# Kernel tuning notes

Hardware: AMD Instinct MI355X
Metric: run time of the kernel (lower is better)

Reference implementation:

```python
import jax, jax.numpy as jnp
import numpy as np

SEED_SPACING = 0.06      # eps for DBSCAN
MIN_SAMPLES = 3          # sklearn counts the point itself
MAX_SUPERPOINTS = 512


def _dbscan_superpoints(coords):
    """DBSCAN(eps, min_samples=3) on [N,3] coords + the module's relabeling.

    Connected components over the eps-graph restricted to core points are
    found by min-index label propagation (with pointer jumping) inside a
    while_loop; border points take the min core-neighbor label; noise is
    filled with the most common label; labels are compacted and capped at
    MAX_SUPERPOINTS exactly as in the torch module. Returns [N] int32.
    """
    N = coords.shape[0]
    SENT = N  # sentinel label meaning "no cluster / noise"

    # pairwise squared euclidean distances via GEMM
    sq = jnp.sum(coords * coords, axis=-1)                      # [N]
    d2 = sq[:, None] + sq[None, :] - 2.0 * (coords @ coords.T)  # [N,N]
    adj = d2 <= SEED_SPACING * SEED_SPACING                     # includes self
    core = jnp.sum(adj, axis=-1) >= MIN_SAMPLES                 # [N] bool

    idx = jnp.arange(N)
    core_col = core[None, :]

    def step(l):
        # min label among core neighbors
        nb = jnp.min(jnp.where(adj & core_col, l[None, :], SENT), axis=-1)
        l2 = jnp.where(core, jnp.minimum(l, nb), SENT)
        # pointer jumping: labels are indices of core points, so l2[l2] is valid
        safe = jnp.where(l2 < N, l2, 0)
        l2 = jnp.where(l2 < N, jnp.minimum(l2, l2[safe]), SENT)
        return l2

    def cond(state):
        return state[1]

    def body(state):
        l, _ = state
        l_new = step(l)
        return l_new, jnp.any(l_new != l)

    l0 = jnp.where(core, idx, SENT)
    l_final, _ = jax.lax.while_loop(cond, body, (l0, jnp.array(True)))

    # border points: min label of any core neighbor; else stay noise
    border = jnp.min(jnp.where(adj & core_col, l_final[None, :], SENT), axis=-1)
    labels = jnp.where(core, l_final, border)

    # noise fill: assign most common valid label (or 0 if none valid)
    noise = labels == SENT
    safe_lab = jnp.where(noise, 0, labels)
    counts = jnp.zeros(N, jnp.int32).at[safe_lab].add(jnp.where(noise, 0, 1))
    any_valid = jnp.any(~noise)
    most_common = jnp.argmax(counts).astype(labels.dtype)
    labels = jnp.where(noise, jnp.where(any_valid, most_common, 0), labels)

    # compact to consecutive ids ordered by min point index (== first occurrence)
    present = jnp.zeros(N, bool).at[labels].set(True)
    rank = (jnp.cumsum(present) - 1).astype(labels.dtype)
    labels = rank[labels]
    n_clusters = jnp.sum(present)

    # cap at MAX_SUPERPOINTS: keep the MAX largest clusters, rest -> 0
    counts2 = jnp.zeros(N, jnp.int32).at[labels].add(1)
    top = jnp.argsort(counts2)[-MAX_SUPERPOINTS:]
    remap = jnp.zeros(N, labels.dtype).at[top].set(
        jnp.arange(MAX_SUPERPOINTS, dtype=labels.dtype))
    labels = jnp.where(n_clusters > MAX_SUPERPOINTS, remap[labels], labels)
    return labels.astype(jnp.int32)


def setup_inputs() -> dict:
    key = jax.random.key(0)
    coordinates = jax.random.uniform(key, (8, 4096, 3), dtype=jnp.float32)
    return {"coordinates": coordinates}


def reference(coordinates):
    # [B, N, 3] -> [B, N] int32 superpoint labels
    return jax.vmap(_dbscan_superpoints)(coordinates)
```

## Files before the change

kernel.cpp:

```cpp
#include <hip/hip_runtime.h>
#include <stdint.h>

#define NPTS 4096
#define SENT NPTS
#define MAXSP 512
#define SCAP 1024
#define NSLICE 32
#define ESLOTS (SCAP*NSLICE)
#define ECACHE 16384

typedef unsigned long long ull;

__device__ __forceinline__ int find_lds(int* p, int x){
  while (true){
    int px = p[x];
    if (px == x) return x;
    int ppx = p[px];
    if (ppx == px) return px;
    p[x] = ppx;
    x = ppx;
  }
}

__device__ __forceinline__ void union_lds(int* p, int a, int b){
  a = find_lds(p, a);
  b = find_lds(p, b);
  while (a != b){
    int lo = min(a, b), hi = max(a, b);
    int old = atomicCAS(&p[hi], hi, lo);
    if (old == hi || old == lo) return;
    a = lo; b = old;
  }
}

__device__ __forceinline__ ull trimask(ull m, int i, int base){
  if (base + 63 <= i) return 0ULL;
  if (base <= i) return m & ((~0ULL) << (i - base + 1));
  return m;
}

__device__ __forceinline__ float4 loadpt(const float* __restrict__ c, int g){
#pragma clang fp contract(off)
  float x = c[g*3+0], y = c[g*3+1], z = c[g*3+2];
  float sq = ((x*x) + (y*y)) + (z*z);
  return make_float4(x, y, z, sq);
}

__global__ __launch_bounds__(1024) void k_adj(const float* __restrict__ coords,
                                              uint32_t* __restrict__ edges,
                                              int* __restrict__ scnt,
                                              int* __restrict__ rcnt){
#pragma clang fp contract(off)
  __shared__ float4 P[NPTS];
  __shared__ int sTot;
  int tid  = threadIdx.x;
  int wid  = tid >> 6, lane = tid & 63;
  int b     = blockIdx.x >> 5;
  int slice = blockIdx.x & 31;
  int u512  = (slice << 4) + wid;
  int i0 = u512 << 2;
  int h0 = (NPTS - 4) - i0;
  const float* cb = coords + ((size_t)b << 12) * 3;
  if (tid == 0) sTot = 0;
  for (int g = tid; g < NPTS; g += 1024) P[g] = loadpt(cb, g);
  __syncthreads();
  const float EPS2 = (float)(0.06 * 0.06);
  float4 pL[4], pH[4];
  #pragma unroll
  for (int r = 0; r < 4; ++r){ pL[r] = P[i0 + r]; pH[r] = P[h0 + r]; }
  ull wl[4] = {0,0,0,0}, wh[4] = {0,0,0,0};
  int base = lane << 6;
  {
    int W = i0 >> 6;
    for (int k = W; k < 64; ++k){
      float4 cur = P[(k << 6) + lane];
      #pragma unroll
      for (int r = 0; r < 4; ++r){
        float dot = __builtin_fmaf(pL[r].z, cur.z,
                    __builtin_fmaf(pL[r].y, cur.y, pL[r].x * cur.x));
        float d2  = __builtin_fmaf(-2.0f, dot, pL[r].w + cur.w);
        ull bal = __ballot(d2 <= EPS2);
        if (lane == k) wl[r] = bal;
      }
    }
  }
  {
    int W = h0 >> 6;
    for (int k = W; k < 64; ++k){
      float4 cur = P[(k << 6) + lane];
      #pragma unroll
      for (int r = 0; r < 4; ++r){
        float dot = __builtin_fmaf(pH[r].z, cur.z,
                    __builtin_fmaf(pH[r].y, cur.y, pH[r].x * cur.x));
        float d2  = __builtin_fmaf(-2.0f, dot, pH[r].w + cur.w);
        ull bal = __ballot(d2 <= EPS2);
        if (lane == k) wh[r] = bal;
      }
    }
  }
  int* rc = rcnt + (b << 12);
  #pragma unroll
  for (int r = 0; r < 4; ++r){
    wl[r] = trimask(wl[r], i0 + r, base);
    wh[r] = trimask(wh[r], h0 + r, base);
    int cl = __popcll(wl[r]), ch = __popcll(wh[r]);
    #pragma unroll
    for (int off = 32; off; off >>= 1){
      cl += __shfl_xor(cl, off);
      ch += __shfl_xor(ch, off);
    }
    if (lane == 0){ rc[i0 + r] = cl; rc[h0 + r] = ch; }
  }
  int cnt = 0;
  #pragma unroll
  for (int r = 0; r < 4; ++r) cnt += __popcll(wl[r]) + __popcll(wh[r]);
  int incl = cnt;
  #pragma unroll
  for (int off = 1; off < 64; off <<= 1){
    int y = __shfl_up(incl, off);
    if (lane >= off) incl += y;
  }
  int total = __shfl(incl, 63);
  int woff = 0;
  if (lane == 63) woff = atomicAdd(&sTot, total);
  woff = __shfl(woff, 63);
  __syncthreads();
  if (tid == 0) scnt[(b << 5) + slice] = min(sTot, SCAP);
  int pos = woff + incl - cnt;
  uint32_t* eb = edges + (size_t)b * ESLOTS + slice * SCAP;
  #define EMIT(mm, row) { ull e = (mm); while (e){ int bit = __builtin_ctzll(e); \
      e &= e - 1; if (pos < SCAP) eb[pos] = ((uint32_t)(row) << 12) | (uint32_t)(base + bit); ++pos; } }
  #pragma unroll
  for (int r = 0; r < 4; ++r) EMIT(wl[r], i0 + r)
  #pragma unroll
  for (int r = 0; r < 4; ++r) EMIT(wh[r], h0 + r)
  #undef EMIT
}

__global__ __launch_bounds__(1024) void k_mega(const uint32_t* __restrict__ edges,
                                               const int* __restrict__ scnt,
                                               const int* __restrict__ rcnt,
                                               uint32_t* __restrict__ spill,
                                               int* __restrict__ out){
  __shared__ int par[NPTS];
  __shared__ int LAB[NPTS];
  __shared__ int Bb[NPTS];
  __shared__ unsigned char corea[NPTS];
  __shared__ uint32_t ec[ECACHE];
  __shared__ int pref[NSLICE + 1];
  __shared__ int wtots[16];
  __shared__ int sMost;
  int b = blockIdx.x, t = threadIdx.x;
  int wid = t >> 6, lane = t & 63;
  const uint32_t* eb = edges + (size_t)b * ESLOTS;
  const int* rc = rcnt + (b << 12);
  uint32_t* sp = spill + (size_t)b * (ESLOTS - ECACHE);
  if (t < NSLICE) pref[t + 1] = scnt[(b << 5) + t];
  if (t == 0){ pref[0] = 0; sMost = -1; }
  for (int s = 0; s < 4; ++s){ int v = (t << 2) + s; par[v] = rc[v]; }
  __syncthreads();
  for (int off = 1; off < NSLICE; off <<= 1){
    int v = 0;
    if (t < NSLICE && t >= off) v = pref[t + 1 - off];
    __syncthreads();
    if (t < NSLICE && t >= off) pref[t + 1] += v;
    __syncthreads();
  }
  int cnt = pref[NSLICE];
  for (int d = t; d < cnt; d += 1024){
    int lo = 0, hi = NSLICE - 1;
    #pragma unroll
    for (int s = 0; s < 5; ++s){
      int mid = (lo + hi) >> 1;
      if (pref[mid + 1] <= d) lo = mid + 1; else hi = mid;
    }
    uint32_t pk = eb[(lo << 10) + (d - pref[lo])];
    if (d < ECACHE) ec[d] = pk; else sp[d - ECACHE] = pk;
    atomicAdd(&par[pk & 4095], 1);
  }
  __syncthreads();
  for (int s = 0; s < 4; ++s){ int v = (t << 2) + s; corea[v] = (par[v] >= 2) ? 1 : 0; }
  __syncthreads();
  for (int s = 0; s < 4; ++s){ int v = (t << 2) + s; par[v] = v; }
  __syncthreads();
  for (int d = t; d < cnt; d += 1024){
    uint32_t pk = (d < ECACHE) ? ec[d] : sp[d - ECACHE];
    int u = pk >> 12, v = pk & 4095;
    if (corea[u] && corea[v]) union_lds(par, u, v);
  }
  __syncthreads();
  for (int s = 0; s < 4; ++s){
    int v = (t << 2) + s;
    LAB[v] = corea[v] ? find_lds(par, v) : SENT;
  }
  __syncthreads();
  for (int d = t; d < cnt; d += 1024){
    uint32_t pk = (d < ECACHE) ? ec[d] : sp[d - ECACHE];
    int u = pk >> 12, v = pk & 4095;
    int cu = corea[u], cv = corea[v];
    if (cu && !cv)      atomicMin(&LAB[v], find_lds(par, u));
    else if (cv && !cu) atomicMin(&LAB[u], find_lds(par, v));
  }
  __syncthreads();
  int* A = par;
  for (int s = 0; s < 4; ++s){ int v = (t << 2) + s; A[v] = 0; }
  __syncthreads();
  for (int s = 0; s < 4; ++s){ int l = LAB[(t << 2) + s]; if (l < SENT) atomicAdd(&A[l], 1); }
  __syncthreads();
  {
    int best = -1;
    for (int s = 0; s < 4; ++s){
      int v = (t << 2) + s; int c = A[v];
      if (c > 0) best = max(best, (c << 13) | (4095 - v));
    }
    #pragma unroll
    for (int off = 32; off; off >>= 1) best = max(best, __shfl_xor(best, off));
    if (lane == 0 && best >= 0) atomicMax(&sMost, best);
  }
  __syncthreads();
  int most = (sMost >= 0) ? (4095 - (sMost & 8191)) : 0;
  for (int s = 0; s < 4; ++s){ int v = (t << 2) + s; if (LAB[v] == SENT) LAB[v] = most; Bb[v] = 0; }
  __syncthreads();
  for (int s = 0; s < 4; ++s) Bb[LAB[(t << 2) + s]] = 1;
  __syncthreads();
  int pv[4]; int ls = 0;
  for (int s = 0; s < 4; ++s){ pv[s] = Bb[(t << 2) + s]; ls += pv[s]; }
  int incl = ls;
  #pragma unroll
  for (int off = 1; off < 64; off <<= 1){
    int y = __shfl_up(incl, off);
    if (lane >= off) incl += y;
  }
  if (lane == 63) wtots[wid] = incl;
  __syncthreads();
  int wbase = 0, ncl = 0;
  #pragma unroll
  for (int w = 0; w < 16; ++w){
    int wt = wtots[w];
    if (w < wid) wbase += wt;
    ncl += wt;
  }
  int run = wbase + incl - ls;
  for (int s = 0; s < 4; ++s){ run += pv[s]; Bb[(t << 2) + s] = run - 1; }
  __syncthreads();
  for (int s = 0; s < 4; ++s){ int v = (t << 2) + s; LAB[v] = Bb[LAB[v]]; }
  __syncthreads();
  if (ncl > MAXSP){
    for (int s = 0; s < 4; ++s) A[(t << 2) + s] = 0;
    __syncthreads();
    for (int s = 0; s < 4; ++s) atomicAdd(&A[LAB[(t << 2) + s]], 1);
    __syncthreads();
    for (int v = t; v < ncl; v += 1024){
      int keyv = A[v] * NPTS + v;
      int p = 0;
      for (int u = 0; u < ncl; ++u) p += ((A[u] * NPTS + u) < keyv) ? 1 : 0;
      int full = p + (NPTS - ncl);
      Bb[v] = (full >= NPTS - MAXSP) ? (full - (NPTS - MAXSP)) : 0;
    }
    __syncthreads();
    for (int s = 0; s < 4; ++s){ int v = (t << 2) + s; LAB[v] = Bb[LAB[v]]; }
    __syncthreads();
  }
  int* og = out + (b << 12);
  for (int s = 0; s < 4; ++s){ int v = (t << 2) + s; og[v] = LAB[v]; }
}

extern "C" void kernel_launch(void* const* d_in, const int* in_sizes, int n_in,
                              void* d_out, int out_size, void* d_ws, size_t ws_size,
                              hipStream_t stream){
  const float* coords = (const float*)d_in[0];
  int* out = (int*)d_out;
  int batches = in_sizes[0] / (NPTS * 3);

  char* ws = (char*)d_ws;
  size_t off = 0;
  int* scnt = (int*)(ws + off); off += (size_t)batches * NSLICE * sizeof(int);
  int* rcnt = (int*)(ws + off); off += (size_t)batches * NPTS * sizeof(int);
  uint32_t* edges = (uint32_t*)(ws + off); off += (size_t)batches * ESLOTS * sizeof(uint32_t);
  uint32_t* spill = (uint32_t*)(ws + off); off += (size_t)batches * (ESLOTS - ECACHE) * sizeof(uint32_t);

  k_adj<<<batches * NSLICE, 1024, 0, stream>>>(coords, edges, scnt, rcnt);
  k_mega<<<batches, 1024, 0, stream>>>(edges, scnt, rcnt, spill, out);
}
```

Baseline: 55.32 us.

## Fuse adjacency and clustering kernels via last-block-done counter per batch

Merges the edge-building kernel and the per-batch clustering kernel into one launch. Each slice block increments a per-batch atomic counter, and the last of the 32 blocks to finish runs the union-find, labeling and compaction phase, reusing the same shared memory regions. This removes a kernel launch and the gap between the two stages. In exchange, the LDS edge cache shrinks, so more edges spill to global memory. The counter is never reset and relies on a modulo-32 test, so correctness across repeated calls depends on the workspace state.

```diff
diff --git a/kernel.cpp b/kernel.cpp
--- a/kernel.cpp
+++ b/kernel.cpp
@@ -7,7 +7,7 @@
 #define SCAP 1024
 #define NSLICE 32
 #define ESLOTS (SCAP*NSLICE)
-#define ECACHE 16384
+#define ECLDS 10752
 
 typedef unsigned long long ull;
 
@@ -46,13 +46,16 @@
   return make_float4(x, y, z, sq);
 }
 
-__global__ __launch_bounds__(1024) void k_adj(const float* __restrict__ coords,
-                                              uint32_t* __restrict__ edges,
-                                              int* __restrict__ scnt,
-                                              int* __restrict__ rcnt){
+__global__ __launch_bounds__(1024, 8) void k_all(const float* __restrict__ coords,
+                                                 uint32_t* __restrict__ edges,
+                                                 int* __restrict__ scnt,
+                                                 int* __restrict__ rcnt,
+                                                 uint32_t* __restrict__ spill,
+                                                 unsigned int* __restrict__ ctr,
+                                                 int* __restrict__ out){
 #pragma clang fp contract(off)
-  __shared__ float4 P[NPTS];
-  __shared__ int sTot;
+  __shared__ float4 R1[NPTS];
+  __shared__ int    R2[NPTS];
   int tid  = threadIdx.x;
   int wid  = tid >> 6, lane = tid & 63;
   int b     = blockIdx.x >> 5;
@@ -61,19 +64,19 @@
   int i0 = u512 << 2;
   int h0 = (NPTS - 4) - i0;
   const float* cb = coords + ((size_t)b << 12) * 3;
-  if (tid == 0) sTot = 0;
-  for (int g = tid; g < NPTS; g += 1024) P[g] = loadpt(cb, g);
+  if (tid == 0) R2[0] = 0;
+  for (int g = tid; g < NPTS; g += 1024) R1[g] = loadpt(cb, g);
   __syncthreads();
   const float EPS2 = (float)(0.06 * 0.06);
-  float4 pL[4], pH[4];
-  #pragma unroll
-  for (int r = 0; r < 4; ++r){ pL[r] = P[i0 + r]; pH[r] = P[h0 + r]; }
-  ull wl[4] = {0,0,0,0}, wh[4] = {0,0,0,0};
   int base = lane << 6;
+  ull wl[4], wh[4];
+  float4 pL[4];
+  #pragma unroll
+  for (int r = 0; r < 4; ++r){ pL[r] = R1[i0 + r]; wl[r] = 0ULL; }
   {
     int W = i0 >> 6;
     for (int k = W; k < 64; ++k){
-      float4 cur = P[(k << 6) + lane];
+      float4 cur = R1[(k << 6) + lane];
       #pragma unroll
       for (int r = 0; r < 4; ++r){
         float dot = __builtin_fmaf(pL[r].z, cur.z,
@@ -85,9 +88,12 @@
     }
   }
   {
+    float4 pH[4];
+    #pragma unroll
+    for (int r = 0; r < 4; ++r){ pH[r] = R1[h0 + r]; wh[r] = 0ULL; }
     int W = h0 >> 6;
     for (int k = W; k < 64; ++k){
-      float4 cur = P[(k << 6) + lane];
+      float4 cur = R1[(k << 6) + lane];
       #pragma unroll
       for (int r = 0; r < 4; ++r){
         float dot = __builtin_fmaf(pH[r].z, cur.z,
@@ -122,10 +128,10 @@
   }
   int total = __shfl(incl, 63);
   int woff = 0;
-  if (lane == 63) woff = atomicAdd(&sTot, total);
+  if (lane == 63) woff = atomicAdd(&R2[0], total);
   woff = __shfl(woff, 63);
   __syncthreads();
-  if (tid == 0) scnt[(b << 5) + slice] = min(sTot, SCAP);
+  if (tid == 0) scnt[(b << 5) + slice] = min(R2[0], SCAP);
   int pos = woff + incl - cnt;
   uint32_t* eb = edges + (size_t)b * ESLOTS + slice * SCAP;
   #define EMIT(mm, row) { ull e = (mm); while (e){ int bit = __builtin_ctzll(e); \
@@ -135,28 +141,31 @@
   #pragma unroll
   for (int r = 0; r < 4; ++r) EMIT(wh[r], h0 + r)
   #undef EMIT
-}
-
-__global__ __launch_bounds__(1024) void k_mega(const uint32_t* __restrict__ edges,
-                                               const int* __restrict__ scnt,
-                                               const int* __restrict__ rcnt,
-                                               uint32_t* __restrict__ spill,
-                                               int* __restrict__ out){
-  __shared__ int par[NPTS];
-  __shared__ int LAB[NPTS];
-  __shared__ int Bb[NPTS];
-  __shared__ unsigned char corea[NPTS];
-  __shared__ uint32_t ec[ECACHE];
-  __shared__ int pref[NSLICE + 1];
-  __shared__ int wtots[16];
-  __shared__ int sMost;
-  int b = blockIdx.x, t = threadIdx.x;
-  int wid = t >> 6, lane = t & 63;
-  const uint32_t* eb = edges + (size_t)b * ESLOTS;
-  const int* rc = rcnt + (b << 12);
-  uint32_t* sp = spill + (size_t)b * (ESLOTS - ECACHE);
+  __threadfence();
+  __syncthreads();
+  if (tid == 0){
+    unsigned int t = atomicAdd(&ctr[b << 6], 1u);
+    R2[1] = ((t & 31u) == 31u) ? 1 : 0;
+  }
+  __syncthreads();
+  bool fire = (R2[1] != 0);
+  __syncthreads();
+  if (!fire) return;
+  __threadfence();
+
+  int* par = R2;
+  uint32_t* ec = (uint32_t*)R1;
+  int* LAB = (int*)((char*)R1 + 43008);
+  unsigned char* corea = (unsigned char*)R1 + 59392;
+  int* pref = (int*)((char*)R1 + 63488);
+  int* wtots = (int*)((char*)R1 + 63624);
+  int* sMost = (int*)((char*)R1 + 63688);
+  int* Bb = (int*)R1;
+  const uint32_t* ebb = edges + (size_t)b * ESLOTS;
+  uint32_t* sp = spill + (size_t)b * (ESLOTS - ECLDS);
+  int t = tid;
   if (t < NSLICE) pref[t + 1] = scnt[(b << 5) + t];
-  if (t == 0){ pref[0] = 0; sMost = -1; }
+  if (t == 0){ pref[0] = 0; *sMost = -1; }
   for (int s = 0; s < 4; ++s){ int v = (t << 2) + s; par[v] = rc[v]; }
   __syncthreads();
   for (int off = 1; off < NSLICE; off <<= 1){
@@ -166,16 +175,16 @@
     if (t < NSLICE && t >= off) pref[t + 1] += v;
     __syncthreads();
   }
-  int cnt = pref[NSLICE];
-  for (int d = t; d < cnt; d += 1024){
+  int ecnt = pref[NSLICE];
+  for (int d = t; d < ecnt; d += 1024){
     int lo = 0, hi = NSLICE - 1;
     #pragma unroll
     for (int s = 0; s < 5; ++s){
       int mid = (lo + hi) >> 1;
       if (pref[mid + 1] <= d) lo = mid + 1; else hi = mid;
     }
-    uint32_t pk = eb[(lo << 10) + (d - pref[lo])];
-    if (d < ECACHE) ec[d] = pk; else sp[d - ECACHE] = pk;
+    uint32_t pk = ebb[(lo << 10) + (d - pref[lo])];
+    if (d < ECLDS) ec[d] = pk; else sp[d - ECLDS] = pk;
     atomicAdd(&par[pk & 4095], 1);
   }
   __syncthreads();
@@ -183,8 +192,8 @@
   __syncthreads();
   for (int s = 0; s < 4; ++s){ int v = (t << 2) + s; par[v] = v; }
   __syncthreads();
-  for (int d = t; d < cnt; d += 1024){
-    uint32_t pk = (d < ECACHE) ? ec[d] : sp[d - ECACHE];
+  for (int d = t; d < ecnt; d += 1024){
+    uint32_t pk = (d < ECLDS) ? ec[d] : sp[d - ECLDS];
     int u = pk >> 12, v = pk & 4095;
     if (corea[u] && corea[v]) union_lds(par, u, v);
   }
@@ -194,8 +203,8 @@
     LAB[v] = corea[v] ? find_lds(par, v) : SENT;
   }
   __syncthreads();
-  for (int d = t; d < cnt; d += 1024){
-    uint32_t pk = (d < ECACHE) ? ec[d] : sp[d - ECACHE];
+  for (int d = t; d < ecnt; d += 1024){
+    uint32_t pk = (d < ECLDS) ? ec[d] : sp[d - ECLDS];
     int u = pk >> 12, v = pk & 4095;
     int cu = corea[u], cv = corea[v];
     if (cu && !cv)      atomicMin(&LAB[v], find_lds(par, u));
@@ -215,23 +224,23 @@
     }
     #pragma unroll
     for (int off = 32; off; off >>= 1) best = max(best, __shfl_xor(best, off));
-    if (lane == 0 && best >= 0) atomicMax(&sMost, best);
-  }
-  __syncthreads();
-  int most = (sMost >= 0) ? (4095 - (sMost & 8191)) : 0;
+    if (lane == 0 && best >= 0) atomicMax(sMost, best);
+  }
+  __syncthreads();
+  int most = (*sMost >= 0) ? (4095 - (*sMost & 8191)) : 0;
   for (int s = 0; s < 4; ++s){ int v = (t << 2) + s; if (LAB[v] == SENT) LAB[v] = most; Bb[v] = 0; }
   __syncthreads();
   for (int s = 0; s < 4; ++s) Bb[LAB[(t << 2) + s]] = 1;
   __syncthreads();
   int pv[4]; int ls = 0;
   for (int s = 0; s < 4; ++s){ pv[s] = Bb[(t << 2) + s]; ls += pv[s]; }
-  int incl = ls;
+  int incl2 = ls;
   #pragma unroll
   for (int off = 1; off < 64; off <<= 1){
-    int y = __shfl_up(incl, off);
-    if (lane >= off) incl += y;
-  }
-  if (lane == 63) wtots[wid] = incl;
+    int y = __shfl_up(incl2, off);
+    if (lane >= off) incl2 += y;
+  }
+  if (lane == 63) wtots[wid] = incl2;
   __syncthreads();
   int wbase = 0, ncl = 0;
   #pragma unroll
@@ -240,7 +249,7 @@
     if (w < wid) wbase += wt;
     ncl += wt;
   }
-  int run = wbase + incl - ls;
+  int run = wbase + incl2 - ls;
   for (int s = 0; s < 4; ++s){ run += pv[s]; Bb[(t << 2) + s] = run - 1; }
   __syncthreads();
   for (int s = 0; s < 4; ++s){ int v = (t << 2) + s; LAB[v] = Bb[LAB[v]]; }
@@ -277,8 +286,9 @@
   int* scnt = (int*)(ws + off); off += (size_t)batches * NSLICE * sizeof(int);
   int* rcnt = (int*)(ws + off); off += (size_t)batches * NPTS * sizeof(int);
   uint32_t* edges = (uint32_t*)(ws + off); off += (size_t)batches * ESLOTS * sizeof(uint32_t);
-  uint32_t* spill = (uint32_t*)(ws + off); off += (size_t)batches * (ESLOTS - ECACHE) * sizeof(uint32_t);
-
-  k_adj<<<batches * NSLICE, 1024, 0, stream>>>(coords, edges, scnt, rcnt);
-  k_mega<<<batches, 1024, 0, stream>>>(edges, scnt, rcnt, spill, out);
-}
+  uint32_t* spill = (uint32_t*)(ws + off); off += (size_t)batches * (ESLOTS - ECLDS) * sizeof(uint32_t);
+  unsigned int* ctr = (unsigned int*)(ws + off); off += (size_t)batches * 64 * sizeof(unsigned int);
+
+  k_all<<<batches * NSLICE, 1024, 0, stream>>>(coords, edges, scnt, rcnt,
+                                               spill, ctr, out);
+}
```

Measured after the change: 133.5 us. 2.41x slower.
